# Performance work log

Hardware: AMD Instinct MI355X
Metric: run time of the kernel (lower is better)

The kernel has to match this reference:

```python
import jax, jax.numpy as jnp
import numpy as np

HIDDEN = 1024
N_EXPERTS = 16
TOP_K = 2
D_FF_EXPERT = 512
D_FF_SHARED = 2048
BATCH, SEQ = 1, 4096


def setup_inputs() -> dict:
    key = jax.random.key(0)
    ks = jax.random.split(key, 8)
    s = 0.02  # init scale to keep router logits sane
    return {
        "x": jax.random.normal(ks[0], (BATCH, SEQ, HIDDEN), dtype=jnp.float32),
        "router_w": jax.random.normal(ks[1], (HIDDEN, N_EXPERTS), dtype=jnp.float32) * s,
        "experts_gate": jax.random.normal(ks[2], (N_EXPERTS, HIDDEN, D_FF_EXPERT), dtype=jnp.float32) * s,
        "experts_up": jax.random.normal(ks[3], (N_EXPERTS, HIDDEN, D_FF_EXPERT), dtype=jnp.float32) * s,
        "experts_down": jax.random.normal(ks[4], (N_EXPERTS, D_FF_EXPERT, HIDDEN), dtype=jnp.float32) * s,
        "shared_gate": jax.random.normal(ks[5], (HIDDEN, D_FF_SHARED), dtype=jnp.float32) * s,
        "shared_up": jax.random.normal(ks[6], (HIDDEN, D_FF_SHARED), dtype=jnp.float32) * s,
        "shared_down": jax.random.normal(ks[7], (D_FF_SHARED, HIDDEN), dtype=jnp.float32) * s,
    }


def reference(x, router_w, experts_gate, experts_up, experts_down,
              shared_gate, shared_up, shared_down):
    B, S, D = x.shape
    T = B * S
    E = experts_gate.shape[0]

    # Shared SwiGLU expert on all tokens: silu(x@Wg) * (x@Wu) @ Wd
    shared_out = (jax.nn.silu(x @ shared_gate) * (x @ shared_up)) @ shared_down  # [B,S,D]

    x_flat = x.reshape(T, D)
    router_probs = jax.nn.softmax(x_flat @ router_w, axis=-1)          # [T,E]
    topk_w, topk_idx = jax.lax.top_k(router_probs, TOP_K)              # [T,k]

    # Combine weights as dense [T,E]; top-k indices are distinct per token,
    # exactly reproducing sum_{i in topk} w_i * expert_i(x).
    combine = jnp.zeros((T, E), x.dtype).at[jnp.arange(T)[:, None], topk_idx].add(topk_w)

    # Per-expert SwiGLU, vectorized over the (small, fixed) expert axis.
    gate = jnp.einsum('td,edf->etf', x_flat, experts_gate)             # [E,T,f]
    up = jnp.einsum('td,edf->etf', x_flat, experts_up)                 # [E,T,f]
    inter = jax.nn.silu(gate) * up                                     # [E,T,f]
    routed = jnp.einsum('etf,efd,te->td', inter, experts_down, combine)  # [T,D]

    return (shared_out.reshape(T, D) + routed).reshape(B, S, D)
```

## Files before the change

### kernel.cpp

```cpp
#include <hip/hip_runtime.h>
#include <hip/hip_bf16.h>
#include <stdint.h>

#define HIDDEN 1024
#define NEXP 16
#define DFF_E 512
#define DFF_S 2048
#define TOKENS 4096
#define NSLOTS 8192

typedef __bf16 bf16x8 __attribute__((ext_vector_type(8)));
typedef float f32x4 __attribute__((ext_vector_type(4)));

__device__ __forceinline__ unsigned short f2bf(float f) {
  unsigned int u = __builtin_bit_cast(unsigned int, f);
  u += 0x7FFFu + ((u >> 16) & 1u);
  return (unsigned short)(u >> 16);
}
__device__ __forceinline__ float bf2f(unsigned short h) {
  unsigned int u = ((unsigned int)h) << 16;
  return __builtin_bit_cast(float, u);
}
__device__ __forceinline__ void gload16(const void* g, void* l) {
  __builtin_amdgcn_global_load_lds(
      (const __attribute__((address_space(1))) unsigned int*)g,
      (__attribute__((address_space(3))) unsigned int*)l, 16, 0, 0);
}

__global__ void router_kernel(const float* __restrict__ x, const float* __restrict__ rw,
                              int* __restrict__ topk_idx, float* __restrict__ topk_w,
                              int* __restrict__ counts) {
  const int t = blockIdx.x;
  const int lane = threadIdx.x;
  float acc[NEXP];
#pragma unroll
  for (int e = 0; e < NEXP; e++) acc[e] = 0.f;
  const float* xr = x + (size_t)t * HIDDEN;
  for (int d = lane; d < HIDDEN; d += 64) {
    const float xv = xr[d];
    const float4* r = (const float4*)(rw + (size_t)d * NEXP);
#pragma unroll
    for (int q = 0; q < 4; q++) {
      float4 rv = r[q];
      acc[q * 4 + 0] += xv * rv.x;
      acc[q * 4 + 1] += xv * rv.y;
      acc[q * 4 + 2] += xv * rv.z;
      acc[q * 4 + 3] += xv * rv.w;
    }
  }
#pragma unroll
  for (int off = 32; off >= 1; off >>= 1)
#pragma unroll
    for (int e = 0; e < NEXP; e++) acc[e] += __shfl_xor(acc[e], off);

  if (lane == 0) {
    float m = acc[0];
#pragma unroll
    for (int e = 1; e < NEXP; e++) m = fmaxf(m, acc[e]);
    float p[NEXP];
    float s = 0.f;
#pragma unroll
    for (int e = 0; e < NEXP; e++) { p[e] = __expf(acc[e] - m); s += p[e]; }
    const float inv = 1.f / s;
    int i0 = 0; float p0 = p[0];
#pragma unroll
    for (int e = 1; e < NEXP; e++) if (p[e] > p0) { p0 = p[e]; i0 = e; }
    int i1 = -1; float p1 = -1.f;
#pragma unroll
    for (int e = 0; e < NEXP; e++) if (e != i0 && p[e] > p1) { p1 = p[e]; i1 = e; }
    topk_idx[t * 2 + 0] = i0;
    topk_idx[t * 2 + 1] = i1;
    topk_w[t * 2 + 0] = p0 * inv;
    topk_w[t * 2 + 1] = p1 * inv;
    atomicAdd(&counts[i0], 1);
    atomicAdd(&counts[i1], 1);
  }
}

__global__ void offsets_kernel(const int* __restrict__ counts, int* __restrict__ offs,
                               int* __restrict__ cursors) {
  if (threadIdx.x == 0) {
    int run = 0;
    for (int e = 0; e < NEXP; e++) { offs[e] = run; run += counts[e]; }
    offs[NEXP] = run;
  }
  if (threadIdx.x < NEXP) cursors[threadIdx.x] = 0;
}

__global__ void build_slots_kernel(const int* __restrict__ topk_idx, const float* __restrict__ topk_w,
                                   const int* __restrict__ offs, int* __restrict__ cursors,
                                   int* __restrict__ slot_token, float* __restrict__ slot_w) {
  const int t = blockIdx.x * blockDim.x + threadIdx.x;
  if (t >= TOKENS) return;
#pragma unroll
  for (int i = 0; i < 2; i++) {
    const int e = topk_idx[t * 2 + i];
    const int pos = atomicAdd(&cursors[e], 1);
    const int slot = offs[e] + pos;
    slot_token[slot] = t;
    slot_w[slot] = topk_w[t * 2 + i];
  }
}

__global__ void convert_kernel(const float* __restrict__ in, unsigned short* __restrict__ out, int n) {
  const int i = (blockIdx.x * blockDim.x + threadIdx.x) * 4;
  if (i >= n) return;
  const float4 v = *(const float4*)(in + i);
  ushort4 o;
  o.x = f2bf(v.x); o.y = f2bf(v.y); o.z = f2bf(v.z); o.w = f2bf(v.w);
  *(ushort4*)(out + i) = o;
}

__global__ void transpose_convert_kernel(const float* __restrict__ in, unsigned short* __restrict__ out,
                                         int K, int N) {
  __shared__ float tile[32][33];
  const int b = blockIdx.z;
  const int k0 = blockIdx.x * 32, n0 = blockIdx.y * 32;
  const float* src = in + (size_t)b * K * N;
  unsigned short* dst = out + (size_t)b * K * N;
  const int tx = threadIdx.x & 31, ty = threadIdx.x >> 5;
#pragma unroll
  for (int r = 0; r < 32; r += 8)
    tile[ty + r][tx] = src[(size_t)(k0 + ty + r) * N + n0 + tx];
  __syncthreads();
#pragma unroll
  for (int r = 0; r < 32; r += 8)
    dst[(size_t)(n0 + ty + r) * K + k0 + tx] = f2bf(tile[tx][ty + r]);
}

__global__ void silu_mul_kernel(const unsigned short* __restrict__ g, const unsigned short* __restrict__ u,
                                unsigned short* __restrict__ out, int n) {
  const int i = (blockIdx.x * blockDim.x + threadIdx.x) * 4;
  if (i >= n) return;
  const ushort4 gv = *(const ushort4*)(g + i);
  const ushort4 uv = *(const ushort4*)(u + i);
  ushort4 o;
  {
    float gf = bf2f(gv.x), uf = bf2f(uv.x);
    o.x = f2bf(gf / (1.f + __expf(-gf)) * uf);
  }
  {
    float gf = bf2f(gv.y), uf = bf2f(uv.y);
    o.y = f2bf(gf / (1.f + __expf(-gf)) * uf);
  }
  {
    float gf = bf2f(gv.z), uf = bf2f(uv.z);
    o.z = f2bf(gf / (1.f + __expf(-gf)) * uf);
  }
  {
    float gf = bf2f(gv.w), uf = bf2f(uv.w);
    o.w = f2bf(gf / (1.f + __expf(-gf)) * uf);
  }
  *(ushort4*)(out + i) = o;
}

__global__ void silu_mul_slots_kernel(const unsigned short* __restrict__ g, const unsigned short* __restrict__ u,
                                      const float* __restrict__ slot_w, unsigned short* __restrict__ out) {
  const int i = (blockIdx.x * blockDim.x + threadIdx.x) * 4;
  if (i >= NSLOTS * DFF_E) return;
  const float w = slot_w[i >> 9];
  const ushort4 gv = *(const ushort4*)(g + i);
  const ushort4 uv = *(const ushort4*)(u + i);
  ushort4 o;
  {
    float gf = bf2f(gv.x), uf = bf2f(uv.x);
    o.x = f2bf(w * gf / (1.f + __expf(-gf)) * uf);
  }
  {
    float gf = bf2f(gv.y), uf = bf2f(uv.y);
    o.y = f2bf(w * gf / (1.f + __expf(-gf)) * uf);
  }
  {
    float gf = bf2f(gv.z), uf = bf2f(uv.z);
    o.z = f2bf(w * gf / (1.f + __expf(-gf)) * uf);
  }
  {
    float gf = bf2f(gv.w), uf = bf2f(uv.w);
    o.w = f2bf(w * gf / (1.f + __expf(-gf)) * uf);
  }
  *(ushort4*)(out + i) = o;
}

template <int MODE>
__global__ __launch_bounds__(256) void gemm_bt_k(const unsigned short* __restrict__ A,
                                                 const unsigned short* __restrict__ B,
                                                 void* __restrict__ Cp, int M, int N, int K,
                                                 const int* __restrict__ offs,
                                                 const int* __restrict__ slot_token) {
  __shared__ __align__(16) unsigned short As[128 * 32];
  __shared__ __align__(16) unsigned short Bs[128 * 32];
  const int tid = threadIdx.x;
  const int lane = tid & 63;
  const int wid = tid >> 6;
  const int wr = wid >> 1, wc = wid & 1;
  const int fr = lane & 15, fq = lane >> 4;

  int rowBase, rowEnd;
  const unsigned short* Bp = B;
  if constexpr (MODE >= 2) {
    const int e = blockIdx.z;
    const int o0 = offs[e], o1 = offs[e + 1];
    rowBase = o0 + blockIdx.x * 128;
    if (rowBase >= o1) return;
    rowEnd = o1;
    Bp += (size_t)e * (size_t)N * (size_t)K;
  } else {
    rowBase = blockIdx.x * 128;
    rowEnd = M;
  }
  const int colBase = blockIdx.y * 128;

  const int rA = tid >> 2;
  const int kOff = (tid & 3) * 8;
  const unsigned short *aRow0, *aRow1;
  {
    const int r0 = rowBase + rA, r1 = rowBase + rA + 64;
    if constexpr (MODE == 2) {
      const int s0 = r0 < NSLOTS ? r0 : NSLOTS - 1;
      const int s1 = r1 < NSLOTS ? r1 : NSLOTS - 1;
      aRow0 = A + (size_t)slot_token[s0] * (size_t)K;
      aRow1 = A + (size_t)slot_token[s1] * (size_t)K;
    } else {
      const int m0 = r0 < M ? r0 : M - 1;
      const int m1 = r1 < M ? r1 : M - 1;
      aRow0 = A + (size_t)m0 * (size_t)K;
      aRow1 = A + (size_t)m1 * (size_t)K;
    }
  }
  const unsigned short* bRow0 = Bp + (size_t)(colBase + rA) * (size_t)K;
  const unsigned short* bRow1 = Bp + (size_t)(colBase + rA + 64) * (size_t)K;

  unsigned short* AsW0 = As + tid * 8;
  unsigned short* AsW1 = As + 2048 + tid * 8;
  unsigned short* BsW0 = Bs + tid * 8;
  unsigned short* BsW1 = Bs + 2048 + tid * 8;

  f32x4 acc[4][4];
#pragma unroll
  for (int i = 0; i < 4; i++)
#pragma unroll
    for (int j = 0; j < 4; j++) acc[i][j] = (f32x4){0.f, 0.f, 0.f, 0.f};

  const unsigned short* AsR = As + (wr * 64 + fr) * 32 + fq * 8;
  const unsigned short* BsR = Bs + (wc * 64 + fr) * 32 + fq * 8;

  for (int k0 = 0; k0 < K; k0 += 32) {
    __syncthreads();
    gload16(aRow0 + k0 + kOff, AsW0);
    gload16(aRow1 + k0 + kOff, AsW1);
    gload16(bRow0 + k0 + kOff, BsW0);
    gload16(bRow1 + k0 + kOff, BsW1);
    __syncthreads();
    bf16x8 af[4], bfr[4];
#pragma unroll
    for (int m = 0; m < 4; m++) af[m] = *(const bf16x8*)(AsR + m * 512);
#pragma unroll
    for (int n = 0; n < 4; n++) bfr[n] = *(const bf16x8*)(BsR + n * 512);
#pragma unroll
    for (int m = 0; m < 4; m++)
#pragma unroll
      for (int n = 0; n < 4; n++)
        acc[m][n] = __builtin_amdgcn_mfma_f32_16x16x32_bf16(af[m], bfr[n], acc[m][n], 0, 0, 0);
  }

#pragma unroll
  for (int m = 0; m < 4; m++) {
    const int rb = rowBase + wr * 64 + m * 16 + fq * 4;
#pragma unroll
    for (int n = 0; n < 4; n++) {
      const int col = colBase + wc * 64 + n * 16 + fr;
#pragma unroll
      for (int j = 0; j < 4; j++) {
        const int r = rb + j;
        if constexpr (MODE >= 2) {
          if (r >= rowEnd) continue;
        }
        const float v = acc[m][n][j];
        if constexpr (MODE == 0) {
          ((unsigned short*)Cp)[(size_t)r * N + col] = f2bf(v);
        } else if constexpr (MODE == 1) {
          ((float*)Cp)[(size_t)r * N + col] = v;
        } else if constexpr (MODE == 2) {
          ((unsigned short*)Cp)[(size_t)r * N + col] = f2bf(v);
        } else {
          const int tok = slot_token[r];
          atomicAdd(((float*)Cp) + (size_t)tok * HIDDEN + col, v);
        }
      }
    }
  }
}

#define WS_XB 0ull
#define WS_WEG 8388608ull
#define WS_WEU 25165824ull
#define WS_WED 41943040ull
#define WS_WSG 58720256ull
#define WS_WSU 62914560ull
#define WS_WSD 67108864ull
#define WS_GBUF 71303168ull
#define WS_UBUF 88080384ull
#define WS_INTERB 104857600ull
#define WS_SLOT_TOKEN 121634816ull
#define WS_SLOT_W 121667584ull
#define WS_TOPK_IDX 121700352ull
#define WS_TOPK_W 121733120ull
#define WS_COUNTS 121765888ull
#define WS_OFFS 121765952ull
#define WS_CURSORS 121766080ull
#define WS_NEEDED 121766144ull

extern "C" void kernel_launch(void* const* d_in, const int* in_sizes, int n_in,
                              void* d_out, int out_size, void* d_ws, size_t ws_size,
                              hipStream_t stream) {
  if (ws_size < WS_NEEDED) return;

  const float* x = (const float*)d_in[0];
  const float* router_w = (const float*)d_in[1];
  const float* eg = (const float*)d_in[2];
  const float* eu = (const float*)d_in[3];
  const float* ed = (const float*)d_in[4];
  const float* sg = (const float*)d_in[5];
  const float* su = (const float*)d_in[6];
  const float* sd = (const float*)d_in[7];

  char* ws = (char*)d_ws;
  unsigned short* xb = (unsigned short*)(ws + WS_XB);
  unsigned short* weg = (unsigned short*)(ws + WS_WEG);
  unsigned short* weu = (unsigned short*)(ws + WS_WEU);
  unsigned short* wed = (unsigned short*)(ws + WS_WED);
  unsigned short* wsg = (unsigned short*)(ws + WS_WSG);
  unsigned short* wsu = (unsigned short*)(ws + WS_WSU);
  unsigned short* wsd = (unsigned short*)(ws + WS_WSD);
  unsigned short* gbuf = (unsigned short*)(ws + WS_GBUF);
  unsigned short* ubuf = (unsigned short*)(ws + WS_UBUF);
  unsigned short* interb = (unsigned short*)(ws + WS_INTERB);
  unsigned short* gslot = (unsigned short*)(ws + WS_GBUF);
  unsigned short* uslot = (unsigned short*)(ws + WS_GBUF + 8388608ull);
  unsigned short* inters = (unsigned short*)(ws + WS_UBUF);
  int* slot_token = (int*)(ws + WS_SLOT_TOKEN);
  float* slot_w = (float*)(ws + WS_SLOT_W);
  int* topk_idx = (int*)(ws + WS_TOPK_IDX);
  float* topk_w = (float*)(ws + WS_TOPK_W);
  int* counts = (int*)(ws + WS_COUNTS);
  int* offs = (int*)(ws + WS_OFFS);
  int* cursors = (int*)(ws + WS_CURSORS);

  float* out = (float*)d_out;

  hipMemsetAsync(counts, 0, NEXP * sizeof(int), stream);
  router_kernel<<<TOKENS, 64, 0, stream>>>(x, router_w, topk_idx, topk_w, counts);
  offsets_kernel<<<1, 64, 0, stream>>>(counts, offs, cursors);
  build_slots_kernel<<<16, 256, 0, stream>>>(topk_idx, topk_w, offs, cursors, slot_token, slot_w);

  convert_kernel<<<4096, 256, 0, stream>>>(x, xb, TOKENS * HIDDEN);
  transpose_convert_kernel<<<dim3(32, 16, 16), 256, 0, stream>>>(eg, weg, 1024, 512);
  transpose_convert_kernel<<<dim3(32, 16, 16), 256, 0, stream>>>(eu, weu, 1024, 512);
  transpose_convert_kernel<<<dim3(16, 32, 16), 256, 0, stream>>>(ed, wed, 512, 1024);
  transpose_convert_kernel<<<dim3(32, 64, 1), 256, 0, stream>>>(sg, wsg, 1024, 2048);
  transpose_convert_kernel<<<dim3(32, 64, 1), 256, 0, stream>>>(su, wsu, 1024, 2048);
  transpose_convert_kernel<<<dim3(64, 32, 1), 256, 0, stream>>>(sd, wsd, 2048, 1024);

  gemm_bt_k<0><<<dim3(32, 16, 1), 256, 0, stream>>>(xb, wsg, gbuf, 4096, 2048, 1024, nullptr, nullptr);
  gemm_bt_k<0><<<dim3(32, 16, 1), 256, 0, stream>>>(xb, wsu, ubuf, 4096, 2048, 1024, nullptr, nullptr);
  silu_mul_kernel<<<8192, 256, 0, stream>>>(gbuf, ubuf, interb, 4096 * 2048);
  gemm_bt_k<1><<<dim3(32, 8, 1), 256, 0, stream>>>(interb, wsd, out, 4096, 1024, 2048, nullptr, nullptr);

  gemm_bt_k<2><<<dim3(32, 4, 16), 256, 0, stream>>>(xb, weg, gslot, NSLOTS, 512, 1024, offs, slot_token);
  gemm_bt_k<2><<<dim3(32, 4, 16), 256, 0, stream>>>(xb, weu, uslot, NSLOTS, 512, 1024, offs, slot_token);
  silu_mul_slots_kernel<<<4096, 256, 0, stream>>>(gslot, uslot, slot_w, inters);
  gemm_bt_k<3><<<dim3(32, 8, 16), 256, 0, stream>>>(inters, wed, out, NSLOTS, 1024, 512, offs, slot_token);
}
```

Baseline: 792.4 us.

## Fuse gate/up GEMMs with SiLU epilogue and replace scatter atomics with combine

```diff
diff --git a/kernel.cpp b/kernel.cpp
--- a/kernel.cpp
+++ b/kernel.cpp
@@ -89,7 +89,8 @@
 
 __global__ void build_slots_kernel(const int* __restrict__ topk_idx, const float* __restrict__ topk_w,
                                    const int* __restrict__ offs, int* __restrict__ cursors,
-                                   int* __restrict__ slot_token, float* __restrict__ slot_w) {
+                                   int* __restrict__ slot_token, float* __restrict__ slot_w,
+                                   int* __restrict__ slot_pos) {
   const int t = blockIdx.x * blockDim.x + threadIdx.x;
   if (t >= TOKENS) return;
 #pragma unroll
@@ -99,6 +100,7 @@
     const int slot = offs[e] + pos;
     slot_token[slot] = t;
     slot_w[slot] = topk_w[t * 2 + i];
+    slot_pos[t * 2 + i] = slot;
   }
 }
 
@@ -128,67 +130,18 @@
     dst[(size_t)(n0 + ty + r) * K + k0 + tx] = f2bf(tile[tx][ty + r]);
 }
 
-__global__ void silu_mul_kernel(const unsigned short* __restrict__ g, const unsigned short* __restrict__ u,
-                                unsigned short* __restrict__ out, int n) {
-  const int i = (blockIdx.x * blockDim.x + threadIdx.x) * 4;
-  if (i >= n) return;
-  const ushort4 gv = *(const ushort4*)(g + i);
-  const ushort4 uv = *(const ushort4*)(u + i);
-  ushort4 o;
-  {
-    float gf = bf2f(gv.x), uf = bf2f(uv.x);
-    o.x = f2bf(gf / (1.f + __expf(-gf)) * uf);
-  }
-  {
-    float gf = bf2f(gv.y), uf = bf2f(uv.y);
-    o.y = f2bf(gf / (1.f + __expf(-gf)) * uf);
-  }
-  {
-    float gf = bf2f(gv.z), uf = bf2f(uv.z);
-    o.z = f2bf(gf / (1.f + __expf(-gf)) * uf);
-  }
-  {
-    float gf = bf2f(gv.w), uf = bf2f(uv.w);
-    o.w = f2bf(gf / (1.f + __expf(-gf)) * uf);
-  }
-  *(ushort4*)(out + i) = o;
-}
-
-__global__ void silu_mul_slots_kernel(const unsigned short* __restrict__ g, const unsigned short* __restrict__ u,
-                                      const float* __restrict__ slot_w, unsigned short* __restrict__ out) {
-  const int i = (blockIdx.x * blockDim.x + threadIdx.x) * 4;
-  if (i >= NSLOTS * DFF_E) return;
-  const float w = slot_w[i >> 9];
-  const ushort4 gv = *(const ushort4*)(g + i);
-  const ushort4 uv = *(const ushort4*)(u + i);
-  ushort4 o;
-  {
-    float gf = bf2f(gv.x), uf = bf2f(uv.x);
-    o.x = f2bf(w * gf / (1.f + __expf(-gf)) * uf);
-  }
-  {
-    float gf = bf2f(gv.y), uf = bf2f(uv.y);
-    o.y = f2bf(w * gf / (1.f + __expf(-gf)) * uf);
-  }
-  {
-    float gf = bf2f(gv.z), uf = bf2f(uv.z);
-    o.z = f2bf(w * gf / (1.f + __expf(-gf)) * uf);
-  }
-  {
-    float gf = bf2f(gv.w), uf = bf2f(uv.w);
-    o.w = f2bf(w * gf / (1.f + __expf(-gf)) * uf);
-  }
-  *(ushort4*)(out + i) = o;
-}
-
-template <int MODE>
-__global__ __launch_bounds__(256) void gemm_bt_k(const unsigned short* __restrict__ A,
-                                                 const unsigned short* __restrict__ B,
-                                                 void* __restrict__ Cp, int M, int N, int K,
-                                                 const int* __restrict__ offs,
-                                                 const int* __restrict__ slot_token) {
+template <int GATHER>
+__global__ __launch_bounds__(256) void fused_gu_k(const unsigned short* __restrict__ A,
+                                                  const unsigned short* __restrict__ Bg,
+                                                  const unsigned short* __restrict__ Bu,
+                                                  unsigned short* __restrict__ C,
+                                                  int M, int N, int K,
+                                                  const int* __restrict__ offs,
+                                                  const int* __restrict__ slot_token,
+                                                  const float* __restrict__ slot_w) {
   __shared__ __align__(16) unsigned short As[128 * 32];
-  __shared__ __align__(16) unsigned short Bs[128 * 32];
+  __shared__ __align__(16) unsigned short Bgs[128 * 32];
+  __shared__ __align__(16) unsigned short Bus[128 * 32];
   const int tid = threadIdx.x;
   const int lane = tid & 63;
   const int wid = tid >> 6;
@@ -196,14 +149,16 @@
   const int fr = lane & 15, fq = lane >> 4;
 
   int rowBase, rowEnd;
-  const unsigned short* Bp = B;
-  if constexpr (MODE >= 2) {
+  const unsigned short* Bgp = Bg;
+  const unsigned short* Bup = Bu;
+  if constexpr (GATHER) {
     const int e = blockIdx.z;
     const int o0 = offs[e], o1 = offs[e + 1];
     rowBase = o0 + blockIdx.x * 128;
     if (rowBase >= o1) return;
     rowEnd = o1;
-    Bp += (size_t)e * (size_t)N * (size_t)K;
+    Bgp += (size_t)e * (size_t)N * (size_t)K;
+    Bup += (size_t)e * (size_t)N * (size_t)K;
   } else {
     rowBase = blockIdx.x * 128;
     rowEnd = M;
@@ -215,7 +170,7 @@
   const unsigned short *aRow0, *aRow1;
   {
     const int r0 = rowBase + rA, r1 = rowBase + rA + 64;
-    if constexpr (MODE == 2) {
+    if constexpr (GATHER) {
       const int s0 = r0 < NSLOTS ? r0 : NSLOTS - 1;
       const int s1 = r1 < NSLOTS ? r1 : NSLOTS - 1;
       aRow0 = A + (size_t)slot_token[s0] * (size_t)K;
@@ -227,14 +182,109 @@
       aRow1 = A + (size_t)m1 * (size_t)K;
     }
   }
+  const unsigned short* bgRow0 = Bgp + (size_t)(colBase + rA) * (size_t)K;
+  const unsigned short* bgRow1 = Bgp + (size_t)(colBase + rA + 64) * (size_t)K;
+  const unsigned short* buRow0 = Bup + (size_t)(colBase + rA) * (size_t)K;
+  const unsigned short* buRow1 = Bup + (size_t)(colBase + rA + 64) * (size_t)K;
+
+  f32x4 accg[4][4], accu[4][4];
+#pragma unroll
+  for (int i = 0; i < 4; i++)
+#pragma unroll
+    for (int j = 0; j < 4; j++) {
+      accg[i][j] = (f32x4){0.f, 0.f, 0.f, 0.f};
+      accu[i][j] = (f32x4){0.f, 0.f, 0.f, 0.f};
+    }
+
+  const unsigned short* AsR = As + (wr * 64 + fr) * 32 + fq * 8;
+  const unsigned short* BgsR = Bgs + (wc * 64 + fr) * 32 + fq * 8;
+  const unsigned short* BusR = Bus + (wc * 64 + fr) * 32 + fq * 8;
+
+  for (int k0 = 0; k0 < K; k0 += 32) {
+    __syncthreads();
+    gload16(aRow0 + k0 + kOff, As + tid * 8);
+    gload16(aRow1 + k0 + kOff, As + 2048 + tid * 8);
+    gload16(bgRow0 + k0 + kOff, Bgs + tid * 8);
+    gload16(bgRow1 + k0 + kOff, Bgs + 2048 + tid * 8);
+    gload16(buRow0 + k0 + kOff, Bus + tid * 8);
+    gload16(buRow1 + k0 + kOff, Bus + 2048 + tid * 8);
+    __syncthreads();
+    bf16x8 af[4], bgf[4], buf[4];
+#pragma unroll
+    for (int m = 0; m < 4; m++) af[m] = *(const bf16x8*)(AsR + m * 512);
+#pragma unroll
+    for (int n = 0; n < 4; n++) bgf[n] = *(const bf16x8*)(BgsR + n * 512);
+#pragma unroll
+    for (int n = 0; n < 4; n++) buf[n] = *(const bf16x8*)(BusR + n * 512);
+#pragma unroll
+    for (int m = 0; m < 4; m++)
+#pragma unroll
+      for (int n = 0; n < 4; n++) {
+        accg[m][n] = __builtin_amdgcn_mfma_f32_16x16x32_bf16(af[m], bgf[n], accg[m][n], 0, 0, 0);
+        accu[m][n] = __builtin_amdgcn_mfma_f32_16x16x32_bf16(af[m], buf[n], accu[m][n], 0, 0, 0);
+      }
+  }
+
+#pragma unroll
+  for (int m = 0; m < 4; m++) {
+    const int rb = rowBase + wr * 64 + m * 16 + fq * 4;
+#pragma unroll
+    for (int n = 0; n < 4; n++) {
+      const int col = colBase + wc * 64 + n * 16 + fr;
+#pragma unroll
+      for (int j = 0; j < 4; j++) {
+        const int r = rb + j;
+        if constexpr (GATHER) {
+          if (r >= rowEnd) continue;
+        }
+        const float g = accg[m][n][j];
+        const float u = accu[m][n][j];
+        float v = g / (1.f + __expf(-g)) * u;
+        if constexpr (GATHER) v *= slot_w[r];
+        C[(size_t)r * N + col] = f2bf(v);
+      }
+    }
+  }
+}
+
+template <int EXPERT>
+__global__ __launch_bounds__(256) void down_gemm_k(const unsigned short* __restrict__ A,
+                                                   const unsigned short* __restrict__ B,
+                                                   void* __restrict__ Cp, int M, int N, int K,
+                                                   const int* __restrict__ offs) {
+  __shared__ __align__(16) unsigned short As[128 * 32];
+  __shared__ __align__(16) unsigned short Bs[128 * 32];
+  const int tid = threadIdx.x;
+  const int lane = tid & 63;
+  const int wid = tid >> 6;
+  const int wr = wid >> 1, wc = wid & 1;
+  const int fr = lane & 15, fq = lane >> 4;
+
+  int rowBase, rowEnd;
+  const unsigned short* Bp = B;
+  if constexpr (EXPERT) {
+    const int e = blockIdx.z;
+    const int o0 = offs[e], o1 = offs[e + 1];
+    rowBase = o0 + blockIdx.x * 128;
+    if (rowBase >= o1) return;
+    rowEnd = o1;
+    Bp += (size_t)e * (size_t)N * (size_t)K;
+  } else {
+    rowBase = blockIdx.x * 128;
+    rowEnd = M;
+  }
+  const int colBase = blockIdx.y * 128;
+
+  const int rA = tid >> 2;
+  const int kOff = (tid & 3) * 8;
+  const int maxRow = (EXPERT ? NSLOTS : M) - 1;
+  const int r0 = min(rowBase + rA, maxRow);
+  const int r1 = min(rowBase + rA + 64, maxRow);
+  const unsigned short* aRow0 = A + (size_t)r0 * (size_t)K;
+  const unsigned short* aRow1 = A + (size_t)r1 * (size_t)K;
   const unsigned short* bRow0 = Bp + (size_t)(colBase + rA) * (size_t)K;
   const unsigned short* bRow1 = Bp + (size_t)(colBase + rA + 64) * (size_t)K;
 
-  unsigned short* AsW0 = As + tid * 8;
-  unsigned short* AsW1 = As + 2048 + tid * 8;
-  unsigned short* BsW0 = Bs + tid * 8;
-  unsigned short* BsW1 = Bs + 2048 + tid * 8;
-
   f32x4 acc[4][4];
 #pragma unroll
   for (int i = 0; i < 4; i++)
@@ -246,10 +296,10 @@
 
   for (int k0 = 0; k0 < K; k0 += 32) {
     __syncthreads();
-    gload16(aRow0 + k0 + kOff, AsW0);
-    gload16(aRow1 + k0 + kOff, AsW1);
-    gload16(bRow0 + k0 + kOff, BsW0);
-    gload16(bRow1 + k0 + kOff, BsW1);
+    gload16(aRow0 + k0 + kOff, As + tid * 8);
+    gload16(aRow1 + k0 + kOff, As + 2048 + tid * 8);
+    gload16(bRow0 + k0 + kOff, Bs + tid * 8);
+    gload16(bRow1 + k0 + kOff, Bs + 2048 + tid * 8);
     __syncthreads();
     bf16x8 af[4], bfr[4];
 #pragma unroll
@@ -272,23 +322,32 @@
 #pragma unroll
       for (int j = 0; j < 4; j++) {
         const int r = rb + j;
-        if constexpr (MODE >= 2) {
+        if constexpr (EXPERT) {
           if (r >= rowEnd) continue;
-        }
-        const float v = acc[m][n][j];
-        if constexpr (MODE == 0) {
-          ((unsigned short*)Cp)[(size_t)r * N + col] = f2bf(v);
-        } else if constexpr (MODE == 1) {
-          ((float*)Cp)[(size_t)r * N + col] = v;
-        } else if constexpr (MODE == 2) {
-          ((unsigned short*)Cp)[(size_t)r * N + col] = f2bf(v);
+          ((unsigned short*)Cp)[(size_t)r * N + col] = f2bf(acc[m][n][j]);
         } else {
-          const int tok = slot_token[r];
-          atomicAdd(((float*)Cp) + (size_t)tok * HIDDEN + col, v);
+          ((float*)Cp)[(size_t)r * N + col] = acc[m][n][j];
         }
       }
     }
   }
+}
+
+__global__ void combine_kernel(float* __restrict__ out, const unsigned short* __restrict__ dslot,
+                               const int* __restrict__ slot_pos) {
+  const int t = blockIdx.x;
+  const int s0 = slot_pos[t * 2 + 0];
+  const int s1 = slot_pos[t * 2 + 1];
+  const int c = threadIdx.x * 4;
+  const ushort4 a = *(const ushort4*)(dslot + (size_t)s0 * HIDDEN + c);
+  const ushort4 b = *(const ushort4*)(dslot + (size_t)s1 * HIDDEN + c);
+  float4* o = (float4*)(out + (size_t)t * HIDDEN + c);
+  float4 v = *o;
+  v.x += bf2f(a.x) + bf2f(b.x);
+  v.y += bf2f(a.y) + bf2f(b.y);
+  v.z += bf2f(a.z) + bf2f(b.z);
+  v.w += bf2f(a.w) + bf2f(b.w);
+  *o = v;
 }
 
 #define WS_XB 0ull
@@ -298,17 +357,18 @@
 #define WS_WSG 58720256ull
 #define WS_WSU 62914560ull
 #define WS_WSD 67108864ull
-#define WS_GBUF 71303168ull
-#define WS_UBUF 88080384ull
-#define WS_INTERB 104857600ull
-#define WS_SLOT_TOKEN 121634816ull
-#define WS_SLOT_W 121667584ull
-#define WS_TOPK_IDX 121700352ull
-#define WS_TOPK_W 121733120ull
-#define WS_COUNTS 121765888ull
-#define WS_OFFS 121765952ull
-#define WS_CURSORS 121766080ull
-#define WS_NEEDED 121766144ull
+#define WS_INTERB 71303168ull
+#define WS_INTERS 88080384ull
+#define WS_DSLOT 96468992ull
+#define WS_SLOT_TOKEN 113246208ull
+#define WS_SLOT_W 113278976ull
+#define WS_SLOT_POS 113311744ull
+#define WS_TOPK_IDX 113344512ull
+#define WS_TOPK_W 113377280ull
+#define WS_COUNTS 113410048ull
+#define WS_OFFS 113410112ull
+#define WS_CURSORS 113410240ull
+#define WS_NEEDED 113410304ull
 
 extern "C" void kernel_launch(void* const* d_in, const int* in_sizes, int n_in,
                               void* d_out, int out_size, void* d_ws, size_t ws_size,
@@ -332,14 +392,12 @@
   unsigned short* wsg = (unsigned short*)(ws + WS_WSG);
   unsigned short* wsu = (unsigned short*)(ws + WS_WSU);
   unsigned short* wsd = (unsigned short*)(ws + WS_WSD);
-  unsigned short* gbuf = (unsigned short*)(ws + WS_GBUF);
-  unsigned short* ubuf = (unsigned short*)(ws + WS_UBUF);
   unsigned short* interb = (unsigned short*)(ws + WS_INTERB);
-  unsigned short* gslot = (unsigned short*)(ws + WS_GBUF);
-  unsigned short* uslot = (unsigned short*)(ws + WS_GBUF + 8388608ull);
-  unsigned short* inters = (unsigned short*)(ws + WS_UBUF);
+  unsigned short* inters = (unsigned short*)(ws + WS_INTERS);
+  unsigned short* dslot = (unsigned short*)(ws + WS_DSLOT);
   int* slot_token = (int*)(ws + WS_SLOT_TOKEN);
   float* slot_w = (float*)(ws + WS_SLOT_W);
+  int* slot_pos = (int*)(ws + WS_SLOT_POS);
   int* topk_idx = (int*)(ws + WS_TOPK_IDX);
   float* topk_w = (float*)(ws + WS_TOPK_W);
   int* counts = (int*)(ws + WS_COUNTS);
@@ -351,7 +409,8 @@
   hipMemsetAsync(counts, 0, NEXP * sizeof(int), stream);
   router_kernel<<<TOKENS, 64, 0, stream>>>(x, router_w, topk_idx, topk_w, counts);
   offsets_kernel<<<1, 64, 0, stream>>>(counts, offs, cursors);
-  build_slots_kernel<<<16, 256, 0, stream>>>(topk_idx, topk_w, offs, cursors, slot_token, slot_w);
+  build_slots_kernel<<<16, 256, 0, stream>>>(topk_idx, topk_w, offs, cursors,
+                                             slot_token, slot_w, slot_pos);
 
   convert_kernel<<<4096, 256, 0, stream>>>(x, xb, TOKENS * HIDDEN);
   transpose_convert_kernel<<<dim3(32, 16, 16), 256, 0, stream>>>(eg, weg, 1024, 512);
@@ -361,13 +420,12 @@
   transpose_convert_kernel<<<dim3(32, 64, 1), 256, 0, stream>>>(su, wsu, 1024, 2048);
   transpose_convert_kernel<<<dim3(64, 32, 1), 256, 0, stream>>>(sd, wsd, 2048, 1024);
 
-  gemm_bt_k<0><<<dim3(32, 16, 1), 256, 0, stream>>>(xb, wsg, gbuf, 4096, 2048, 1024, nullptr, nullptr);
-  gemm_bt_k<0><<<dim3(32, 16, 1), 256, 0, stream>>>(xb, wsu, ubuf, 4096, 2048, 1024, nullptr, nullptr);
-  silu_mul_kernel<<<8192, 256, 0, stream>>>(gbuf, ubuf, interb, 4096 * 2048);
-  gemm_bt_k<1><<<dim3(32, 8, 1), 256, 0, stream>>>(interb, wsd, out, 4096, 1024, 2048, nullptr, nullptr);
-
-  gemm_bt_k<2><<<dim3(32, 4, 16), 256, 0, stream>>>(xb, weg, gslot, NSLOTS, 512, 1024, offs, slot_token);
-  gemm_bt_k<2><<<dim3(32, 4, 16), 256, 0, stream>>>(xb, weu, uslot, NSLOTS, 512, 1024, offs, slot_token);
-  silu_mul_slots_kernel<<<4096, 256, 0, stream>>>(gslot, uslot, slot_w, inters);
-  gemm_bt_k<3><<<dim3(32, 8, 16), 256, 0, stream>>>(inters, wed, out, NSLOTS, 1024, 512, offs, slot_token);
-}
+  fused_gu_k<0><<<dim3(32, 16, 1), 256, 0, stream>>>(xb, wsg, wsu, interb, TOKENS, DFF_S, HIDDEN,
+                                                     nullptr, nullptr, nullptr);
+  down_gemm_k<0><<<dim3(32, 8, 1), 256, 0, stream>>>(interb, wsd, out, TOKENS, HIDDEN, DFF_S, nullptr);
+
+  fused_gu_k<1><<<dim3(16, 4, 16), 256, 0, stream>>>(xb, weg, weu, inters, NSLOTS, DFF_E, HIDDEN,
+                                                     offs, slot_token, slot_w);
+  down_gemm_k<1><<<dim3(16, 8, 16), 256, 0, stream>>>(inters, wed, dslot, NSLOTS, HIDDEN, DFF_E, offs);
+  combine_kernel<<<TOKENS, 256, 0, stream>>>(out, dslot, slot_pos);
+}
```

Result: faster. 684.9 us (-13.6%).
